# Optimization experiments

Measured on AMD Instinct MI355X. Metric: run time of the kernel, lower is better.

Reference implementation:

```python
import jax, jax.numpy as jnp
import numpy as np

# Hyperparameters (from HOIMLoss init_kwargs / defaults)
NUM_PIDS = 5532
NUM_CQ = 5000
NUM_BG = 5000
NUM_FEATURES = 256
BATCH = 4096
OIM_SCALAR = 30.0
ALPHA_D = 0.25
ALPHA_R = 0.25
GAMMA_D = 2.0
GAMMA_R = 2.0


def _l2norm(x):
    return x / jnp.maximum(jnp.linalg.norm(x, axis=-1, keepdims=True), 1e-12)


def setup_inputs() -> dict:
    key = jax.random.key(0)
    k1, k2, k3, k4, k5 = jax.random.split(key, 5)
    inputs = _l2norm(jax.random.normal(k1, (BATCH, NUM_FEATURES), dtype=jnp.float32))
    # roi_label: -2 = background, -1 = ignored unlabeled, [0, NUM_PIDS) = identity
    roi_label = jax.random.randint(k2, (BATCH,), -2, NUM_PIDS)
    lut = _l2norm(jax.random.normal(k3, (NUM_PIDS, NUM_FEATURES), dtype=jnp.float32))
    cq = _l2norm(jax.random.normal(k4, (NUM_CQ, NUM_FEATURES), dtype=jnp.float32))
    cqb = _l2norm(jax.random.normal(k5, (NUM_BG, NUM_FEATURES), dtype=jnp.float32))
    return {"inputs": inputs, "roi_label": roi_label, "lut": lut, "cq": cq, "cqb": cqb}


def reference(inputs, roi_label, lut, cq, cqb):
    # OIM2CQ.forward: concat([inputs@cqb.T, inputs@lut.T, inputs@cq.T], dim=1)
    table = jnp.concatenate([cqb, lut, cq], axis=0)        # [BG+P+CQ, F]
    projected = OIM_SCALAR * (inputs @ table.T)            # [B, BG+P+CQ]

    valid = roi_label >= -1      # non-background rows (inds in torch code)
    labeled = roi_label >= 0     # rows contributing to nll (ignore_index=-1)

    # OIM focal loss over non-background columns [labeled | unlabeled]
    proj_non_bg = projected[:, NUM_BG:]                    # [B, P+CQ]
    logp = jax.nn.log_softmax(proj_non_bg, axis=-1)
    p = jnp.exp(logp)
    focal_p = ALPHA_R * (1.0 - p) ** GAMMA_R * logp
    safe_lab = jnp.clip(roi_label, 0, NUM_PIDS - 1)
    row_loss = -jnp.take_along_axis(focal_p, safe_lab[:, None], axis=1)[:, 0]
    row_loss = jnp.where(labeled, row_loss, 0.0)           # ignore_index=-1 -> 0

    # Detection focal loss over (background, foreground) mass
    all_probs = jax.nn.softmax(projected, axis=-1)
    cls_score = jnp.stack(
        [all_probs[:, :NUM_BG].sum(axis=-1), all_probs[:, NUM_BG:].sum(axis=-1)],
        axis=-1,
    )                                                      # [B, 2]
    det_label = jnp.clip(roi_label + 2, 0, 1)              # -2 -> 0, else 1
    focal_det = ALPHA_D * (1.0 - cls_score) ** GAMMA_D * jnp.log(cls_score)
    loss_det = -jnp.take_along_axis(focal_det, det_label[:, None], axis=1)[:, 0].mean()

    # dynamic_lambda: weight per-row oim loss by detached fg prob squared
    cls_non_bg = jax.lax.stop_gradient(cls_score[:, 1])
    row_loss = row_loss * cls_non_bg ** 2
    n_valid = jnp.maximum(valid.sum(), 1).astype(projected.dtype)
    loss_oim = jnp.sum(jnp.where(valid, row_loss, 0.0)) / n_valid

    return cls_score, loss_det, loss_oim
```

## Files before the change

kernel.cpp:

```cpp
#include <hip/hip_runtime.h>
#include <hip/hip_bf16.h>

typedef unsigned short u16;
typedef __attribute__((ext_vector_type(8))) short bf16x8;
typedef __attribute__((ext_vector_type(4))) short bf16x4;
typedef __attribute__((ext_vector_type(4))) float f32x4;

#define NBG   5000
#define NPID  5532
#define NTOT  15532
#define FEAT  256
#define BATCH 4096
#define SCALE_LOG2E 43.280851226668994f
#define LPITCH 264

#define NTILE_B  976
#define TILE_SH  4096
#define NTILE_A  256

#define TABT_BYTES ((size_t)NTILE_B * TILE_SH * 2)
#define AT_BYTES   ((size_t)NTILE_A * TILE_SH * 2)
#define SUMS_OFF   (TABT_BYTES + AT_BYTES)
#define SUMS_FLOATS 8196
#define WS_NEED    (SUMS_OFF + SUMS_FLOATS * 4)

__device__ __forceinline__ void atomic_add_f(float* p, float v) {
    __hip_atomic_fetch_add(p, v, __ATOMIC_RELAXED, __HIP_MEMORY_SCOPE_AGENT);
}
__device__ __forceinline__ short f2bf(float f) {
    return (short)__bfloat16_as_ushort(__float2bfloat16(f));
}

__device__ __forceinline__ const float* table_row(
    int n, const float* __restrict__ lut, const float* __restrict__ cq,
    const float* __restrict__ cqb)
{
    const int nc = n < NTOT ? n : NTOT - 1;
    if (nc < NBG)        return cqb + (size_t)nc * FEAT;
    if (nc < NBG + NPID) return lut + (size_t)(nc - NBG) * FEAT;
    return cq + (size_t)(nc - NBG - NPID) * FEAT;
}

#define TAB_UNITS (NTILE_B * 512)
#define A_UNITS   (NTILE_A * 512)
#define PRE_BLOCKS ((TAB_UNITS + A_UNITS) / 256)

__global__ __launch_bounds__(256) void prepass_kernel(
    const float* __restrict__ inputs, const float* __restrict__ lut,
    const float* __restrict__ cq, const float* __restrict__ cqb,
    u16* __restrict__ tabt, u16* __restrict__ at, float* __restrict__ S)
{
    const int u = blockIdx.x * 256 + threadIdx.x;
    if (u < SUMS_FLOATS) S[u] = 0.f;

    if (u < TAB_UNITS) {
        const int tile = u >> 9, v = u & 511;
        const int kk = v >> 6, col = (v >> 2) & 15, q = v & 3;
        const int cg = tile * 16 + col;
        bf16x8 r = {0, 0, 0, 0, 0, 0, 0, 0};
        if (cg < NTOT) {
            const float* src = table_row(cg, lut, cq, cqb) + kk * 32 + q * 8;
            const f32x4 lo = *(const f32x4*)src;
            const f32x4 hi = *(const f32x4*)(src + 4);
            r = bf16x8{ f2bf(lo[0]), f2bf(lo[1]), f2bf(lo[2]), f2bf(lo[3]),
                        f2bf(hi[0]), f2bf(hi[1]), f2bf(hi[2]), f2bf(hi[3]) };
        }
        *(bf16x8*)(tabt + (size_t)u * 8) = r;
    } else {
        const int ua = u - TAB_UNITS;
        const int tile = ua >> 9, v = ua & 511;
        const int kk = v >> 6, row = (v >> 2) & 15, q = v & 3;
        const float* src = inputs + (size_t)(tile * 16 + row) * FEAT + kk * 32 + q * 8;
        const f32x4 lo = *(const f32x4*)src;
        const f32x4 hi = *(const f32x4*)(src + 4);
        bf16x8 r = { f2bf(lo[0]), f2bf(lo[1]), f2bf(lo[2]), f2bf(lo[3]),
                     f2bf(hi[0]), f2bf(hi[1]), f2bf(hi[2]), f2bf(hi[3]) };
        *(bf16x8*)(at + (size_t)ua * 8) = r;
    }
}

__global__ __launch_bounds__(256, 2) void score_bf16_kernel(
    const u16* __restrict__ tabt, const u16* __restrict__ at,
    float* __restrict__ sum_bg, float* __restrict__ sum_nb)
{
    __shared__ __align__(16) short lbuf[2][TILE_SH];
    const int lid = blockIdx.x;
    const int x8  = lid & 7;
    const int j   = lid >> 3;
    const int rowchunk = x8 * 2 + (j & 1);
    const int colchunk = j >> 1;

    const int tid  = threadIdx.x;
    const int wave = tid >> 6;
    const int lane = tid & 63;
    const int l15  = lane & 15;
    const int quad = lane >> 4;

    bf16x8 af[4][8];
    {
        const u16* ab = at + (size_t)(rowchunk * 16 + wave * 4) * TILE_SH
                           + l15 * 32 + quad * 8;
        #pragma unroll
        for (int s = 0; s < 4; ++s)
            #pragma unroll
            for (int kk = 0; kk < 8; ++kk)
                af[s][kk] = *(const bf16x8*)(ab + (size_t)s * TILE_SH + kk * 512);
    }

    float pbg[16], pnb[16];
    #pragma unroll
    for (int i = 0; i < 16; ++i) { pbg[i] = 0.f; pnb[i] = 0.f; }

    const int bt0  = colchunk * 16;
    const int tmax = (colchunk == 60) ? 11 : 16;

    bf16x8 r0, r1;
    {
        const u16* g = tabt + (size_t)bt0 * TILE_SH;
        r0 = *(const bf16x8*)(g + tid * 8);
        r1 = *(const bf16x8*)(g + 2048 + tid * 8);
    }

    #pragma unroll 1
    for (int t = 0; t < tmax; ++t) {
        const int bt = bt0 + t;
        {
            short* dst = lbuf[t & 1];
            *(bf16x8*)(dst + tid * 8) = r0;
            *(bf16x8*)(dst + 2048 + tid * 8) = r1;
        }
        if (t + 1 < tmax) {
            const u16* g = tabt + (size_t)(bt + 1) * TILE_SH;
            r0 = *(const bf16x8*)(g + tid * 8);
            r1 = *(const bf16x8*)(g + 2048 + tid * 8);
        }
        __syncthreads();

        const short* lb = lbuf[t & 1];
        f32x4 cc[4];
        #pragma unroll
        for (int s = 0; s < 4; ++s) cc[s] = f32x4{0.f, 0.f, 0.f, 0.f};
        #pragma unroll
        for (int kk = 0; kk < 8; ++kk) {
            const bf16x8 b = *(const bf16x8*)(lb + kk * 512 + l15 * 32 + quad * 8);
            cc[0] = __builtin_amdgcn_mfma_f32_16x16x32_bf16(af[0][kk], b, cc[0], 0, 0, 0);
            cc[1] = __builtin_amdgcn_mfma_f32_16x16x32_bf16(af[1][kk], b, cc[1], 0, 0, 0);
            cc[2] = __builtin_amdgcn_mfma_f32_16x16x32_bf16(af[2][kk], b, cc[2], 0, 0, 0);
            cc[3] = __builtin_amdgcn_mfma_f32_16x16x32_bf16(af[3][kk], b, cc[3], 0, 0, 0);
        }

        if (colchunk != 60) {
            if (bt < 312) {
                #pragma unroll
                for (int s = 0; s < 4; ++s)
                    #pragma unroll
                    for (int r = 0; r < 4; ++r)
                        pbg[s * 4 + r] += exp2f(cc[s][r] * SCALE_LOG2E);
            } else if (bt > 312) {
                #pragma unroll
                for (int s = 0; s < 4; ++s)
                    #pragma unroll
                    for (int r = 0; r < 4; ++r)
                        pnb[s * 4 + r] += exp2f(cc[s][r] * SCALE_LOG2E);
            } else {
                const bool isbg = l15 < 8;
                #pragma unroll
                for (int s = 0; s < 4; ++s)
                    #pragma unroll
                    for (int r = 0; r < 4; ++r) {
                        const float e = exp2f(cc[s][r] * SCALE_LOG2E);
                        pbg[s * 4 + r] += isbg ? e : 0.f;
                        pnb[s * 4 + r] += isbg ? 0.f : e;
                    }
            }
        } else {
            const bool okc = (bt * 16 + l15) < NTOT;
            #pragma unroll
            for (int s = 0; s < 4; ++s)
                #pragma unroll
                for (int r = 0; r < 4; ++r) {
                    const float e = exp2f(cc[s][r] * SCALE_LOG2E);
                    pnb[s * 4 + r] += okc ? e : 0.f;
                }
        }
    }

    #pragma unroll
    for (int off = 1; off < 16; off <<= 1) {
        #pragma unroll
        for (int i = 0; i < 16; ++i) {
            pbg[i] += __shfl_xor(pbg[i], off);
            pnb[i] += __shfl_xor(pnb[i], off);
        }
    }
    if (l15 == 0) {
        #pragma unroll
        for (int s = 0; s < 4; ++s) {
            #pragma unroll
            for (int r = 0; r < 4; ++r) {
                const int row = (rowchunk * 16 + wave * 4 + s) * 16 + quad * 4 + r;
                atomic_add_f(&sum_bg[row], pbg[s * 4 + r]);
                atomic_add_f(&sum_nb[row], pnb[s * 4 + r]);
            }
        }
    }
}

__global__ __launch_bounds__(256, 2) void score_f32_kernel(
    const float* __restrict__ inputs, const float* __restrict__ lut,
    const float* __restrict__ cq, const float* __restrict__ cqb,
    float* __restrict__ sum_bg, float* __restrict__ sum_nb)
{
    __shared__ __align__(16) short lds[32 * LPITCH];
    const int wave = threadIdx.x >> 6;
    const int lane = threadIdx.x & 63;
    const int l15  = lane & 15;
    const int quad = lane >> 4;
    const int rowbase = blockIdx.y * 256;
    const int colbase = blockIdx.x * 256;

    bf16x8 afrag[4][8];
    #pragma unroll 1
    for (int c = 0; c < 8; ++c) {
        __syncthreads();
        #pragma unroll
        for (int i = 0; i < 8; ++i) {
            const int lr = i * 4 + wave;
            const f32x4 v = *(const f32x4*)(inputs + (size_t)(rowbase + c * 32 + lr) * FEAT + lane * 4);
            bf16x4 h = { f2bf(v[0]), f2bf(v[1]), f2bf(v[2]), f2bf(v[3]) };
            *(bf16x4*)(&lds[lr * LPITCH + lane * 4]) = h;
        }
        __syncthreads();
        if ((c >> 1) == wave) {
            const int half = c & 1;
            #pragma unroll
            for (int j2 = 0; j2 < 2; ++j2) {
                const int lr = j2 * 16 + l15;
                #pragma unroll
                for (int kk = 0; kk < 8; ++kk)
                    afrag[half * 2 + j2][kk] =
                        *(const bf16x8*)(&lds[lr * LPITCH + kk * 32 + quad * 8]);
            }
        }
    }

    float pbg[16], pnb[16];
    #pragma unroll
    for (int i = 0; i < 16; ++i) { pbg[i] = 0.f; pnb[i] = 0.f; }

    #pragma unroll 1
    for (int s = 0; s < 8; ++s) {
        __syncthreads();
        #pragma unroll
        for (int i = 0; i < 8; ++i) {
            const int lc = i * 4 + wave;
            const f32x4 v = *(const f32x4*)(table_row(colbase + s * 32 + lc, lut, cq, cqb) + lane * 4);
            bf16x4 h = { f2bf(v[0]), f2bf(v[1]), f2bf(v[2]), f2bf(v[3]) };
            *(bf16x4*)(&lds[lc * LPITCH + lane * 4]) = h;
        }
        __syncthreads();

        #pragma unroll
        for (int st = 0; st < 2; ++st) {
            const int lc = st * 16 + l15;
            f32x4 cc[4];
            #pragma unroll
            for (int q = 0; q < 4; ++q) cc[q] = f32x4{0.f, 0.f, 0.f, 0.f};
            #pragma unroll
            for (int kk = 0; kk < 8; ++kk) {
                const bf16x8 b = *(const bf16x8*)(&lds[lc * LPITCH + kk * 32 + quad * 8]);
                cc[0] = __builtin_amdgcn_mfma_f32_16x16x32_bf16(afrag[0][kk], b, cc[0], 0, 0, 0);
                cc[1] = __builtin_amdgcn_mfma_f32_16x16x32_bf16(afrag[1][kk], b, cc[1], 0, 0, 0);
                cc[2] = __builtin_amdgcn_mfma_f32_16x16x32_bf16(afrag[2][kk], b, cc[2], 0, 0, 0);
                cc[3] = __builtin_amdgcn_mfma_f32_16x16x32_bf16(afrag[3][kk], b, cc[3], 0, 0, 0);
            }
            const int n = colbase + s * 32 + st * 16 + l15;
            const bool okc  = n < NTOT;
            const bool isbg = n < NBG;
            #pragma unroll
            for (int q = 0; q < 4; ++q) {
                #pragma unroll
                for (int r = 0; r < 4; ++r) {
                    float e = exp2f(cc[q][r] * SCALE_LOG2E);
                    e = okc ? e : 0.f;
                    pbg[q * 4 + r] += isbg ? e : 0.f;
                    pnb[q * 4 + r] += isbg ? 0.f : e;
                }
            }
        }
    }

    #pragma unroll
    for (int off = 1; off < 16; off <<= 1) {
        #pragma unroll
        for (int i = 0; i < 16; ++i) {
            pbg[i] += __shfl_xor(pbg[i], off);
            pnb[i] += __shfl_xor(pnb[i], off);
        }
    }
    if (l15 == 0) {
        #pragma unroll
        for (int q = 0; q < 4; ++q) {
            #pragma unroll
            for (int r = 0; r < 4; ++r) {
                const int row = rowbase + wave * 64 + q * 16 + quad * 4 + r;
                atomic_add_f(&sum_bg[row], pbg[q * 4 + r]);
                atomic_add_f(&sum_nb[row], pnb[q * 4 + r]);
            }
        }
    }
}

__global__ __launch_bounds__(256) void finalize_kernel(
    const float* __restrict__ inputs, const int* __restrict__ roi_label,
    const float* __restrict__ lut,
    const float* __restrict__ sum_bg, const float* __restrict__ sum_nb,
    float* __restrict__ accums, unsigned int* __restrict__ ticket,
    float* __restrict__ out)
{
    __shared__ float s_det[4], s_oim[4], s_nv[4];
    const int wid  = threadIdx.x >> 6;
    const int lane = threadIdx.x & 63;

    float det_a = 0.f, oim_a = 0.f, nv_a = 0.f;

    #pragma unroll 1
    for (int it = 0; it < 8; ++it) {
        const int row = blockIdx.x * 32 + wid * 8 + it;
        const int r   = roi_label[row];

        float dot = 0.f;
        {
            const int rc = r < 0 ? 0 : r;
            const f32x4 xi = *(const f32x4*)(inputs + (size_t)row * FEAT + lane * 4);
            const f32x4 li = *(const f32x4*)(lut + (size_t)rc * FEAT + lane * 4);
            #pragma unroll
            for (int jj = 0; jj < 4; ++jj) {
                float a = __bfloat162float(__float2bfloat16(xi[jj]));
                float b = __bfloat162float(__float2bfloat16(li[jj]));
                dot += a * b;
            }
        }
        #pragma unroll
        for (int off = 32; off > 0; off >>= 1) dot += __shfl_xor(dot, off);

        if (lane == 0) {
            const float sbg = sum_bg[row];
            const float snb = sum_nb[row];
            const float inv = 1.f / (sbg + snb);
            const float cls0 = sbg * inv;
            const float cls1 = snb * inv;
            out[2 * row]     = cls0;
            out[2 * row + 1] = cls1;

            const float cs = (r >= -1) ? cls1 : cls0;
            const float om = 1.f - cs;
            det_a += -(0.25f * om * om * logf(cs)) * (1.f / (float)BATCH);
            nv_a  += (r >= -1) ? 1.f : 0.f;

            if (r >= 0) {
                const float slab = 30.f * dot;
                const float logp = slab - logf(snb);
                const float p    = expf(logp);
                const float om2  = 1.f - p;
                oim_a += -(0.25f * om2 * om2 * logp) * cls1 * cls1;
            }
        }
    }

    if (lane == 0) { s_det[wid] = det_a; s_oim[wid] = oim_a; s_nv[wid] = nv_a; }
    __syncthreads();
    if (threadIdx.x == 0) {
        atomic_add_f(&accums[0], s_det[0] + s_det[1] + s_det[2] + s_det[3]);
        atomic_add_f(&accums[1], s_oim[0] + s_oim[1] + s_oim[2] + s_oim[3]);
        atomic_add_f(&accums[2], s_nv[0] + s_nv[1] + s_nv[2] + s_nv[3]);
        __threadfence();
        const unsigned t = __hip_atomic_fetch_add(ticket, 1u, __ATOMIC_ACQ_REL,
                                                  __HIP_MEMORY_SCOPE_AGENT);
        if (t == gridDim.x - 1) {
            const float det = __hip_atomic_load(&accums[0], __ATOMIC_RELAXED, __HIP_MEMORY_SCOPE_AGENT);
            const float oim = __hip_atomic_load(&accums[1], __ATOMIC_RELAXED, __HIP_MEMORY_SCOPE_AGENT);
            float nv        = __hip_atomic_load(&accums[2], __ATOMIC_RELAXED, __HIP_MEMORY_SCOPE_AGENT);
            if (nv < 1.f) nv = 1.f;
            out[2 * BATCH]     = det;
            out[2 * BATCH + 1] = oim / nv;
        }
    }
}

extern "C" void kernel_launch(void* const* d_in, const int* in_sizes, int n_in,
                              void* d_out, int out_size, void* d_ws, size_t ws_size,
                              hipStream_t stream)
{
    const float* inputs = (const float*)d_in[0];
    const int*   roi    = (const int*)d_in[1];
    const float* lut    = (const float*)d_in[2];
    const float* cq     = (const float*)d_in[3];
    const float* cqb    = (const float*)d_in[4];
    float* out = (float*)d_out;

    if (ws_size >= (size_t)WS_NEED) {
        u16* tabt = (u16*)d_ws;
        u16* at   = (u16*)((char*)d_ws + TABT_BYTES);
        float* S  = (float*)((char*)d_ws + SUMS_OFF);
        prepass_kernel<<<PRE_BLOCKS, 256, 0, stream>>>(inputs, lut, cq, cqb, tabt, at, S);
        score_bf16_kernel<<<976, 256, 0, stream>>>(tabt, at, S, S + BATCH);
        finalize_kernel<<<128, 256, 0, stream>>>(
            inputs, roi, lut, S, S + BATCH, S + 2 * BATCH,
            (unsigned int*)(S + 2 * BATCH + 3), out);
    } else {
        float* S = (float*)d_ws;
        hipMemsetAsync(S, 0, SUMS_FLOATS * sizeof(float), stream);
        dim3 g1(61, 16);
        score_f32_kernel<<<g1, 256, 0, stream>>>(inputs, lut, cq, cqb, S, S + BATCH);
        finalize_kernel<<<128, 256, 0, stream>>>(
            inputs, roi, lut, S, S + BATCH, S + 2 * BATCH,
            (unsigned int*)(S + 2 * BATCH + 3), out);
    }
}
```

Before: 139.9 us.

## Fuse finalize into score kernel and deepen tile prefetch with swizzled layout

Removes the separate finalize launch. Each row chunk now counts its finished blocks, and the last block to finish computes the per-row losses using the bf16 copies already in the workspace. The prefetch pipeline now keeps two tiles in flight in registers instead of one. The bf16 tile layout changes so each lane reads a contiguous 16-byte chunk, which may reduce LDS bank conflicts. The cost is extra registers for the deeper prefetch and a serialized tail block per row chunk.

```diff
diff --git a/kernel.cpp b/kernel.cpp
--- a/kernel.cpp
+++ b/kernel.cpp
@@ -2,6 +2,7 @@
 #include <hip/hip_bf16.h>
 
 typedef unsigned short u16;
+typedef unsigned int u32;
 typedef __attribute__((ext_vector_type(8))) short bf16x8;
 typedef __attribute__((ext_vector_type(4))) short bf16x4;
 typedef __attribute__((ext_vector_type(4))) float f32x4;
@@ -21,14 +22,20 @@
 #define TABT_BYTES ((size_t)NTILE_B * TILE_SH * 2)
 #define AT_BYTES   ((size_t)NTILE_A * TILE_SH * 2)
 #define SUMS_OFF   (TABT_BYTES + AT_BYTES)
-#define SUMS_FLOATS 8196
+#define SUMS_FLOATS 8212
 #define WS_NEED    (SUMS_OFF + SUMS_FLOATS * 4)
 
 __device__ __forceinline__ void atomic_add_f(float* p, float v) {
     __hip_atomic_fetch_add(p, v, __ATOMIC_RELAXED, __HIP_MEMORY_SCOPE_AGENT);
 }
+__device__ __forceinline__ float atomic_ld_f(const float* p) {
+    return __hip_atomic_load(p, __ATOMIC_RELAXED, __HIP_MEMORY_SCOPE_AGENT);
+}
 __device__ __forceinline__ short f2bf(float f) {
     return (short)__bfloat16_as_ushort(__float2bfloat16(f));
+}
+__device__ __forceinline__ float bf2f(u16 u) {
+    union { u32 i; float f; } v; v.i = ((u32)u) << 16; return v.f;
 }
 
 __device__ __forceinline__ const float* table_row(
@@ -55,7 +62,7 @@
 
     if (u < TAB_UNITS) {
         const int tile = u >> 9, v = u & 511;
-        const int kk = v >> 6, col = (v >> 2) & 15, q = v & 3;
+        const int kk = v >> 6, q = (v >> 4) & 3, col = v & 15;
         const int cg = tile * 16 + col;
         bf16x8 r = {0, 0, 0, 0, 0, 0, 0, 0};
         if (cg < NTOT) {
@@ -69,7 +76,7 @@
     } else {
         const int ua = u - TAB_UNITS;
         const int tile = ua >> 9, v = ua & 511;
-        const int kk = v >> 6, row = (v >> 2) & 15, q = v & 3;
+        const int kk = v >> 6, q = (v >> 4) & 3, row = v & 15;
         const float* src = inputs + (size_t)(tile * 16 + row) * FEAT + kk * 32 + q * 8;
         const f32x4 lo = *(const f32x4*)src;
         const f32x4 hi = *(const f32x4*)(src + 4);
@@ -81,9 +88,19 @@
 
 __global__ __launch_bounds__(256, 2) void score_bf16_kernel(
     const u16* __restrict__ tabt, const u16* __restrict__ at,
-    float* __restrict__ sum_bg, float* __restrict__ sum_nb)
+    const int* __restrict__ roi, float* __restrict__ S,
+    float* __restrict__ out)
 {
     __shared__ __align__(16) short lbuf[2][TILE_SH];
+    __shared__ float red[12];
+    __shared__ u32 sflag;
+
+    float* sum_bg = S;
+    float* sum_nb = S + BATCH;
+    float* acc    = S + 2 * BATCH;
+    u32*   gt     = (u32*)(S + 2 * BATCH + 3);
+    u32*   rct    = (u32*)(S + 2 * BATCH + 4);
+
     const int lid = blockIdx.x;
     const int x8  = lid & 7;
     const int j   = lid >> 3;
@@ -99,7 +116,7 @@
     bf16x8 af[4][8];
     {
         const u16* ab = at + (size_t)(rowchunk * 16 + wave * 4) * TILE_SH
-                           + l15 * 32 + quad * 8;
+                           + quad * 128 + l15 * 8;
         #pragma unroll
         for (int s = 0; s < 4; ++s)
             #pragma unroll
@@ -114,35 +131,39 @@
     const int bt0  = colchunk * 16;
     const int tmax = (colchunk == 60) ? 11 : 16;
 
-    bf16x8 r0, r1;
+    bf16x8 rg[2][2];
     {
         const u16* g = tabt + (size_t)bt0 * TILE_SH;
-        r0 = *(const bf16x8*)(g + tid * 8);
-        r1 = *(const bf16x8*)(g + 2048 + tid * 8);
+        rg[0][0] = *(const bf16x8*)(g + tid * 8);
+        rg[0][1] = *(const bf16x8*)(g + 2048 + tid * 8);
+        const u16* g1 = g + TILE_SH;
+        rg[1][0] = *(const bf16x8*)(g1 + tid * 8);
+        rg[1][1] = *(const bf16x8*)(g1 + 2048 + tid * 8);
     }
 
     #pragma unroll 1
     for (int t = 0; t < tmax; ++t) {
-        const int bt = bt0 + t;
+        const int bt  = bt0 + t;
+        const int sel = t & 1;
         {
-            short* dst = lbuf[t & 1];
-            *(bf16x8*)(dst + tid * 8) = r0;
-            *(bf16x8*)(dst + 2048 + tid * 8) = r1;
-        }
-        if (t + 1 < tmax) {
-            const u16* g = tabt + (size_t)(bt + 1) * TILE_SH;
-            r0 = *(const bf16x8*)(g + tid * 8);
-            r1 = *(const bf16x8*)(g + 2048 + tid * 8);
+            short* dst = lbuf[sel];
+            *(bf16x8*)(dst + tid * 8) = rg[sel][0];
+            *(bf16x8*)(dst + 2048 + tid * 8) = rg[sel][1];
+        }
+        if (t + 2 < tmax) {
+            const u16* g = tabt + (size_t)(bt + 2) * TILE_SH;
+            rg[sel][0] = *(const bf16x8*)(g + tid * 8);
+            rg[sel][1] = *(const bf16x8*)(g + 2048 + tid * 8);
         }
         __syncthreads();
 
-        const short* lb = lbuf[t & 1];
+        const short* lb = lbuf[sel];
         f32x4 cc[4];
         #pragma unroll
         for (int s = 0; s < 4; ++s) cc[s] = f32x4{0.f, 0.f, 0.f, 0.f};
         #pragma unroll
         for (int kk = 0; kk < 8; ++kk) {
-            const bf16x8 b = *(const bf16x8*)(lb + kk * 512 + l15 * 32 + quad * 8);
+            const bf16x8 b = *(const bf16x8*)(lb + kk * 512 + quad * 128 + l15 * 8);
             cc[0] = __builtin_amdgcn_mfma_f32_16x16x32_bf16(af[0][kk], b, cc[0], 0, 0, 0);
             cc[1] = __builtin_amdgcn_mfma_f32_16x16x32_bf16(af[1][kk], b, cc[1], 0, 0, 0);
             cc[2] = __builtin_amdgcn_mfma_f32_16x16x32_bf16(af[2][kk], b, cc[2], 0, 0, 0);
@@ -204,6 +225,77 @@
             }
         }
     }
+
+    __syncthreads();
+    if (tid == 0) {
+        __threadfence();
+        const u32 tt = __hip_atomic_fetch_add(&rct[rowchunk], 1u,
+                                              __ATOMIC_ACQ_REL, __HIP_MEMORY_SCOPE_AGENT);
+        sflag = (tt == 60) ? 1u : 0u;
+    }
+    __syncthreads();
+    if (sflag) {
+        const int row = rowchunk * 256 + tid;
+        const int r   = roi[row];
+
+        const int lr = NBG + (r < 0 ? 0 : r);
+        const u16* arow = at   + (size_t)(row >> 4) * TILE_SH + (row & 15) * 8;
+        const u16* brow = tabt + (size_t)(lr  >> 4) * TILE_SH + (lr  & 15) * 8;
+        float dot = 0.f;
+        #pragma unroll 4
+        for (int c = 0; c < 32; ++c) {
+            const bf16x8 av = *(const bf16x8*)(arow + c * 128);
+            const bf16x8 bv = *(const bf16x8*)(brow + c * 128);
+            #pragma unroll
+            for (int jj = 0; jj < 8; ++jj)
+                dot += bf2f((u16)av[jj]) * bf2f((u16)bv[jj]);
+        }
+
+        const float sbg = atomic_ld_f(&sum_bg[row]);
+        const float snb = atomic_ld_f(&sum_nb[row]);
+        const float inv = 1.f / (sbg + snb);
+        const float cls0 = sbg * inv;
+        const float cls1 = snb * inv;
+        out[2 * row]     = cls0;
+        out[2 * row + 1] = cls1;
+
+        const float cs = (r >= -1) ? cls1 : cls0;
+        const float om = 1.f - cs;
+        float det_c = -(0.25f * om * om * logf(cs)) * (1.f / (float)BATCH);
+        float nv_c  = (r >= -1) ? 1.f : 0.f;
+        float oim_c = 0.f;
+        if (r >= 0) {
+            const float logp = 30.f * dot - logf(snb);
+            const float p    = expf(logp);
+            const float om2  = 1.f - p;
+            oim_c = -(0.25f * om2 * om2 * logp) * cls1 * cls1;
+        }
+
+        #pragma unroll
+        for (int off = 32; off > 0; off >>= 1) {
+            det_c += __shfl_xor(det_c, off);
+            oim_c += __shfl_xor(oim_c, off);
+            nv_c  += __shfl_xor(nv_c,  off);
+        }
+        if (lane == 0) { red[wave*3] = det_c; red[wave*3+1] = oim_c; red[wave*3+2] = nv_c; }
+        __syncthreads();
+        if (tid == 0) {
+            atomic_add_f(&acc[0], red[0] + red[3] + red[6] + red[9]);
+            atomic_add_f(&acc[1], red[1] + red[4] + red[7] + red[10]);
+            atomic_add_f(&acc[2], red[2] + red[5] + red[8] + red[11]);
+            __threadfence();
+            const u32 g = __hip_atomic_fetch_add(gt, 1u, __ATOMIC_ACQ_REL,
+                                                 __HIP_MEMORY_SCOPE_AGENT);
+            if (g == 15) {
+                const float det = atomic_ld_f(&acc[0]);
+                const float oim = atomic_ld_f(&acc[1]);
+                float nv        = atomic_ld_f(&acc[2]);
+                if (nv < 1.f) nv = 1.f;
+                out[2 * BATCH]     = det;
+                out[2 * BATCH + 1] = oim / nv;
+            }
+        }
+    }
 }
 
 __global__ __launch_bounds__(256, 2) void score_f32_kernel(
@@ -335,11 +427,8 @@
             const f32x4 xi = *(const f32x4*)(inputs + (size_t)row * FEAT + lane * 4);
             const f32x4 li = *(const f32x4*)(lut + (size_t)rc * FEAT + lane * 4);
             #pragma unroll
-            for (int jj = 0; jj < 4; ++jj) {
-                float a = __bfloat162float(__float2bfloat16(xi[jj]));
-                float b = __bfloat162float(__float2bfloat16(li[jj]));
-                dot += a * b;
-            }
+            for (int jj = 0; jj < 4; ++jj)
+                dot += bf2f((u16)f2bf(xi[jj])) * bf2f((u16)f2bf(li[jj]));
         }
         #pragma unroll
         for (int off = 32; off > 0; off >>= 1) dot += __shfl_xor(dot, off);
@@ -359,8 +448,7 @@
             nv_a  += (r >= -1) ? 1.f : 0.f;
 
             if (r >= 0) {
-                const float slab = 30.f * dot;
-                const float logp = slab - logf(snb);
+                const float logp = 30.f * dot - logf(snb);
                 const float p    = expf(logp);
                 const float om2  = 1.f - p;
                 oim_a += -(0.25f * om2 * om2 * logp) * cls1 * cls1;
@@ -378,9 +466,9 @@
         const unsigned t = __hip_atomic_fetch_add(ticket, 1u, __ATOMIC_ACQ_REL,
                                                   __HIP_MEMORY_SCOPE_AGENT);
         if (t == gridDim.x - 1) {
-            const float det = __hip_atomic_load(&accums[0], __ATOMIC_RELAXED, __HIP_MEMORY_SCOPE_AGENT);
-            const float oim = __hip_atomic_load(&accums[1], __ATOMIC_RELAXED, __HIP_MEMORY_SCOPE_AGENT);
-            float nv        = __hip_atomic_load(&accums[2], __ATOMIC_RELAXED, __HIP_MEMORY_SCOPE_AGENT);
+            const float det = atomic_ld_f(&accums[0]);
+            const float oim = atomic_ld_f(&accums[1]);
+            float nv        = atomic_ld_f(&accums[2]);
             if (nv < 1.f) nv = 1.f;
             out[2 * BATCH]     = det;
             out[2 * BATCH + 1] = oim / nv;
@@ -404,10 +492,7 @@
         u16* at   = (u16*)((char*)d_ws + TABT_BYTES);
         float* S  = (float*)((char*)d_ws + SUMS_OFF);
         prepass_kernel<<<PRE_BLOCKS, 256, 0, stream>>>(inputs, lut, cq, cqb, tabt, at, S);
-        score_bf16_kernel<<<976, 256, 0, stream>>>(tabt, at, S, S + BATCH);
-        finalize_kernel<<<128, 256, 0, stream>>>(
-            inputs, roi, lut, S, S + BATCH, S + 2 * BATCH,
-            (unsigned int*)(S + 2 * BATCH + 3), out);
+        score_bf16_kernel<<<976, 256, 0, stream>>>(tabt, at, roi, S, out);
     } else {
         float* S = (float*)d_ws;
         hipMemsetAsync(S, 0, SUMS_FLOATS * sizeof(float), stream);
```

Measured after the change: 544.8 us. 289% more time.
